# Kernel optimization log

Hardware: AMD Instinct MI355X
Metric: run time of the kernel (lower is better)

## Reference

```python
import jax, jax.numpy as jnp
import numpy as np

N_ENT = 50000
N_REL = 500
IN_DIM = 128
OUT_DIM = 128
N_EDGES = 500000
LRELU_SLOPE = 0.01  # torch F.leaky_relu default


def setup_inputs() -> dict:
    key = jax.random.key(0)
    ks = jax.random.split(key, 8)
    # triplets [3, E]: row0=src entity, row1=relation, row2=dst entity.
    # Ensure every entity appears as a source so no 0/0 in the edge-softmax division.
    src_extra = jax.random.randint(ks[0], (N_EDGES - N_ENT,), 0, N_ENT)
    src = jnp.concatenate([jnp.arange(N_ENT), src_extra])
    rel = jax.random.randint(ks[1], (N_EDGES,), 0, N_REL)
    dst = jax.random.randint(ks[2], (N_EDGES,), 0, N_ENT)
    triplets = jnp.stack([src, rel, dst]).astype(jnp.int64)
    ent_embed = jax.random.normal(ks[3], (N_ENT, IN_DIM), dtype=jnp.float32)
    rel_embed = jax.random.normal(ks[4], (N_REL, IN_DIM), dtype=jnp.float32)
    adj = jax.random.randint(ks[5], (2, N_EDGES), 0, N_ENT).astype(jnp.int64)  # unused by forward
    # Xavier-normal (gain=1.414) init for the two linear layers, like the torch module.
    std_a = 1.414 * np.sqrt(2.0 / (3 * IN_DIM + OUT_DIM))
    std_a2 = 1.414 * np.sqrt(2.0 / (OUT_DIM + 1))
    W_a = jax.random.normal(ks[6], (3 * IN_DIM, OUT_DIM), dtype=jnp.float32) * std_a
    b_a = jnp.zeros((OUT_DIM,), dtype=jnp.float32)
    W_a2 = jax.random.normal(ks[7], (OUT_DIM, 1), dtype=jnp.float32) * std_a2
    b_a2 = jnp.zeros((1,), dtype=jnp.float32)
    return {"triplets": triplets, "ent_embed": ent_embed, "rel_embed": rel_embed,
            "adj": adj, "W_a": W_a, "b_a": b_a, "W_a2": W_a2, "b_a2": b_a2}


def reference(triplets, ent_embed, rel_embed, adj, W_a, b_a, W_a2, b_a2):
    src, rel, dst = triplets[0], triplets[1], triplets[2]
    n_ent = ent_embed.shape[0]
    # Gather + concat: [E, 3*in_dim]
    h = jnp.concatenate([ent_embed[src], rel_embed[rel], ent_embed[dst]], axis=1)
    c = h @ W_a + b_a                                   # [E, out_dim]
    b = jax.nn.leaky_relu(c @ W_a2 + b_a2, LRELU_SLOPE)  # [E, 1]
    e_b = jnp.exp(b)                                    # [E, 1]
    # Sparse edge-softmax grouped by source node (sparse.sum over dst dim).
    denom = jax.ops.segment_sum(e_b, src, num_segments=n_ent)        # [N, 1]
    numer = jax.ops.segment_sum(e_b * c, src, num_segments=n_ent)    # [N, out_dim]
    out = numer / denom
    return jax.nn.elu(out)  # concat=True branch
```

## Files before the change

kernel.cpp:

```cpp
#include <hip/hip_runtime.h>

#define DIM 128

typedef __attribute__((ext_vector_type(8))) short bf16x8;
typedef __attribute__((ext_vector_type(4))) float f32x4;

__device__ inline unsigned short to_bf16(float f) {
    unsigned u = __float_as_uint(f);
    u = (u + 0x7FFFu + ((u >> 16) & 1u)) >> 16;
    return (unsigned short)u;
}
__device__ inline unsigned pack_bf16(float lo, float hi) {
    return (unsigned)to_bf16(lo) | ((unsigned)to_bf16(hi) << 16);
}
__device__ inline float unpack_lo(unsigned v) { return __uint_as_float(v << 16); }
__device__ inline float unpack_hi(unsigned v) { return __uint_as_float(v & 0xFFFF0000u); }

__global__ void wprep_kernel(const float* __restrict__ W_a, unsigned short* __restrict__ Wt,
                             int* __restrict__ counts, int n) {
    const int c = blockIdx.x;
    const int k = threadIdx.x;
    const int srow = (c < 128) ? k : (256 + k);
    const int scol = (c < 128) ? c : (c - 128);
    Wt[c * DIM + k] = to_bf16(W_a[srow * DIM + scol]);
    for (int i = blockIdx.x * 128 + k; i < n; i += 256 * 128) counts[i] = 0;
}

__global__ __launch_bounds__(256, 4) void stage1_kernel(
        const float* __restrict__ ent, const float* __restrict__ rel,
        const int* __restrict__ T, const unsigned short* __restrict__ Wt,
        const float* __restrict__ W_rel, const float* __restrict__ b_a,
        const float* __restrict__ Wa2,
        unsigned* __restrict__ P1h, unsigned* __restrict__ P3h, unsigned* __restrict__ P2h,
        float* __restrict__ q1, float* __restrict__ q3, float* __restrict__ q2,
        int* __restrict__ counts, int NE, int NR, int E, int GB, int HB, int RB) {
    __shared__ unsigned smem[8320];
    int b = blockIdx.x;
    const int t = threadIdx.x;

    if (b < GB) {
        const int half = b & 1;
        const int mrow = (b >> 1) * 128;

        #pragma unroll 4
        for (int i = 0; i < 16; ++i) {
            const int idx = i * 256 + t;
            const int row = idx >> 5;
            const int f4  = idx & 31;
            const int rg  = min(mrow + row, NE - 1);
            const float4 u = *(const float4*)(ent + (size_t)rg * DIM + f4 * 4);
            const unsigned d0 = pack_bf16(u.x, u.y);
            const unsigned d1 = pack_bf16(u.z, u.w);
            const int dw = (f4 * 2) ^ ((row & 7) << 2);
            *(uint2*)&smem[row * 64 + dw] = make_uint2(d0, d1);
        }
        __syncthreads();

        const int wv = t >> 6, lane = t & 63;
        const int g = lane >> 4, m = lane & 15;
        const unsigned short* Wh = Wt + half * 128 * DIM;

        f32x4 acc[2][8];
        #pragma unroll
        for (int rt = 0; rt < 2; ++rt)
            #pragma unroll
            for (int ct = 0; ct < 8; ++ct) acc[rt][ct] = (f32x4){0.f, 0.f, 0.f, 0.f};

        #pragma unroll
        for (int kk = 0; kk < 4; ++kk) {
            const int dwa = (kk * 16 + g * 4) ^ ((m & 7) << 2);
            const bf16x8 a0 = *(const bf16x8*)&smem[(wv * 32 + m) * 64 + dwa];
            const bf16x8 a1 = *(const bf16x8*)&smem[(wv * 32 + 16 + m) * 64 + dwa];
            #pragma unroll
            for (int ct = 0; ct < 8; ++ct) {
                const bf16x8 bb = *(const bf16x8*)(Wh + (ct * 16 + m) * DIM + kk * 32 + g * 8);
                acc[0][ct] = __builtin_amdgcn_mfma_f32_16x16x32_bf16(a0, bb, acc[0][ct], 0, 0, 0);
                acc[1][ct] = __builtin_amdgcn_mfma_f32_16x16x32_bf16(a1, bb, acc[1][ct], 0, 0, 0);
            }
        }
        __syncthreads();

        unsigned* __restrict__ Ph = half ? P3h : P1h;
        float*    __restrict__ qo = half ? q3  : q1;
        unsigned short* lds16 = (unsigned short*)smem;

        #pragma unroll
        for (int rt = 0; rt < 2; ++rt) {
            float qp[4] = {0.f, 0.f, 0.f, 0.f};
            #pragma unroll
            for (int ct = 0; ct < 8; ++ct) {
                const int c = ct * 16 + m;
                const float bias = half ? 0.0f : b_a[c];
                const float wa2  = Wa2[c];
                #pragma unroll
                for (int r = 0; r < 4; ++r) {
                    const float v = acc[rt][ct][r] + bias;
                    qp[r] += v * wa2;
                    lds16[(wv * 32 + rt * 16 + g * 4 + r) * 130 + c] = to_bf16(v);
                }
            }
            #pragma unroll
            for (int r = 0; r < 4; ++r) {
                float v = qp[r];
                #pragma unroll
                for (int o = 1; o < 16; o <<= 1) v += __shfl_xor(v, o);
                const int row = mrow + wv * 32 + rt * 16 + g * 4 + r;
                if (m == 0 && row < NE) qo[row] = v;
            }
        }
        __syncthreads();
        for (int i = 0; i < 32; ++i) {
            const int linear = i * 256 + t;
            const int row = linear >> 6, d = linear & 63;
            const int rg = mrow + row;
            if (rg < NE) Ph[(size_t)rg * 64 + d] = smem[row * 65 + d];
        }
        return;
    }
    b -= GB;

    if (b < HB) {
        for (int e = b * 256 + t; e < E; e += HB * 256)
            atomicAdd(&counts[T[e]], 1);
        return;
    }
    b -= HB;

    {
        float* xs   = (float*)smem;
        float* sred = (float*)(smem + 1024);
        const int row0 = b * 8;
        const int half = t >> 7;
        const int tc   = t & 127;
        #pragma unroll
        for (int e = 0; e < 4; ++e) {
            int row = row0 + half * 4 + e;
            xs[(half * 4 + e) * DIM + tc] = (row < NR) ? rel[(size_t)row * DIM + tc] : 0.0f;
        }
        __syncthreads();
        float acc[4] = {0.f, 0.f, 0.f, 0.f};
        #pragma unroll 4
        for (int k = 0; k < DIM; ++k) {
            const float wv = W_rel[k * DIM + tc];
            #pragma unroll
            for (int e = 0; e < 4; ++e) acc[e] += xs[(half * 4 + e) * DIM + k] * wv;
        }
        const float wa2 = Wa2[tc];
        const int lane = t & 63;
        #pragma unroll
        for (int e = 0; e < 4; ++e) {
            float v = acc[e] * wa2;
            #pragma unroll
            for (int o = 32; o > 0; o >>= 1) v += __shfl_down(v, o);
            if (lane == 0) sred[(half * 4 + e) * 2 + ((t >> 6) & 1)] = v;
        }
        __syncthreads();
        #pragma unroll
        for (int e = 0; e < 4; ++e) {
            int row = row0 + half * 4 + e;
            float hi = __shfl_down(acc[e], 1);
            if (row < NR && (tc & 1) == 0)
                P2h[(size_t)row * 64 + (tc >> 1)] = pack_bf16(acc[e], hi);
        }
        if (t < 8) {
            int row = row0 + t;
            if (row < NR) q2[row] = sred[t * 2] + sred[t * 2 + 1];
        }
    }
}

__device__ inline int wave_incl_scan(int v) {
    const int lane = threadIdx.x & 63;
    #pragma unroll
    for (int o = 1; o < 64; o <<= 1) {
        int u = __shfl_up(v, o);
        if (lane >= o) v += u;
    }
    return v;
}

__global__ void scan_bsum_kernel(const int* __restrict__ counts, int* __restrict__ bsum, int n) {
    const int t = threadIdx.x;
    const int base = blockIdx.x * 1024 + t * 4;
    int s = 0;
    #pragma unroll
    for (int j = 0; j < 4; ++j) if (base + j < n) s += counts[base + j];
    #pragma unroll
    for (int o = 32; o > 0; o >>= 1) s += __shfl_down(s, o);
    __shared__ int ws[4];
    if ((t & 63) == 0) ws[t >> 6] = s;
    __syncthreads();
    if (t == 0) bsum[blockIdx.x] = ws[0] + ws[1] + ws[2] + ws[3];
}

__global__ void scan_write_kernel(const int* __restrict__ counts, const int* __restrict__ bsum,
                                  int* __restrict__ offsets, int* __restrict__ cursor,
                                  int n, int total, int nb) {
    __shared__ int s_boff;
    __shared__ int wsum[4], wpre[4];
    const int t = threadIdx.x;
    if (t < 64) {
        int v = (t < nb) ? bsum[t] : 0;
        int incl = wave_incl_scan(v);
        int ex = incl - v;
        int want = __shfl(ex, (int)blockIdx.x);
        if (t == 0) s_boff = want;
    }
    const int base = blockIdx.x * 1024 + t * 4;
    int c[4];
    int s = 0;
    #pragma unroll
    for (int j = 0; j < 4; ++j) {
        c[j] = (base + j < n) ? counts[base + j] : 0;
        s += c[j];
    }
    int incl = wave_incl_scan(s);
    const int wid = t >> 6, lane = t & 63;
    if (lane == 63) wsum[wid] = incl;
    __syncthreads();
    if (t == 0) {
        int run = 0;
        #pragma unroll
        for (int k = 0; k < 4; ++k) { wpre[k] = run; run += wsum[k]; }
    }
    __syncthreads();
    int run = incl - s + wpre[wid] + s_boff;
    #pragma unroll
    for (int j = 0; j < 4; ++j) {
        if (base + j < n) { offsets[base + j] = run; cursor[base + j] = run; run += c[j]; }
    }
    if (base == 0 && blockIdx.x == 0) offsets[n] = total;
}

__global__ void scatter_kernel(const int* __restrict__ T, const float* __restrict__ q1,
                               const float* __restrict__ q2, const float* __restrict__ q3,
                               const float* __restrict__ b_a2, int* __restrict__ cursor,
                               uint2* __restrict__ rdw, int E) {
    const int e = blockIdx.x * blockDim.x + threadIdx.x;
    if (e >= E) return;
    const int s = T[e], r = T[E + e], d = T[2 * E + e];
    float b = q1[s] + q2[r] + q3[d] + b_a2[0];
    b = (b > 0.0f) ? b : 0.01f * b;
    const float wv = __expf(b);
    const int pos = atomicAdd(&cursor[s], 1);
    rdw[pos] = make_uint2(((unsigned)r << 17) | (unsigned)d, __float_as_uint(wv));
}

__global__ void gather_kernel(const int* __restrict__ offsets, const uint2* __restrict__ rdw,
                              const unsigned* __restrict__ P1h, const unsigned* __restrict__ P2h,
                              const unsigned* __restrict__ P3h, float* __restrict__ out, int n) {
    const int node = (blockIdx.x << 2) + (threadIdx.x >> 6);
    if (node >= n) return;
    const int lane = threadIdx.x & 63;
    const int lo = offsets[node], hi = offsets[node + 1];
    float axp[4] = {0.f,0.f,0.f,0.f};
    float ayp[4] = {0.f,0.f,0.f,0.f};
    float wsp[4] = {0.f,0.f,0.f,0.f};
    int i = lo;
    for (; i + 3 < hi; i += 4) {
        uint2 e[4];
        #pragma unroll
        for (int j = 0; j < 4; ++j) e[j] = rdw[i + j];
        unsigned v2[4], v3[4];
        #pragma unroll
        for (int j = 0; j < 4; ++j) {
            v2[j] = P2h[(size_t)(e[j].x >> 17) * 64 + lane];
            v3[j] = P3h[(size_t)(e[j].x & 0x1FFFFu) * 64 + lane];
        }
        #pragma unroll
        for (int j = 0; j < 4; ++j) {
            const float wv = __uint_as_float(e[j].y);
            axp[j] += wv * (unpack_lo(v2[j]) + unpack_lo(v3[j]));
            ayp[j] += wv * (unpack_hi(v2[j]) + unpack_hi(v3[j]));
            wsp[j] += wv;
        }
    }
    for (; i < hi; ++i) {
        const uint2 e0 = rdw[i];
        const unsigned v2a = P2h[(size_t)(e0.x >> 17) * 64 + lane];
        const unsigned v3a = P3h[(size_t)(e0.x & 0x1FFFFu) * 64 + lane];
        const float wv = __uint_as_float(e0.y);
        axp[0] += wv * (unpack_lo(v2a) + unpack_lo(v3a));
        ayp[0] += wv * (unpack_hi(v2a) + unpack_hi(v3a));
        wsp[0] += wv;
    }
    const float ax = (axp[0] + axp[1]) + (axp[2] + axp[3]);
    const float ay = (ayp[0] + ayp[1]) + (ayp[2] + ayp[3]);
    const float inv = 1.0f / ((wsp[0] + wsp[1]) + (wsp[2] + wsp[3]));
    const unsigned p1 = P1h[(size_t)node * 64 + lane];
    float v0 = unpack_lo(p1) + ax * inv;
    float v1 = unpack_hi(p1) + ay * inv;
    v0 = (v0 > 0.0f) ? v0 : (__expf(v0) - 1.0f);
    v1 = (v1 > 0.0f) ? v1 : (__expf(v1) - 1.0f);
    *(float2*)(out + (size_t)node * DIM + (lane << 1)) = make_float2(v0, v1);
}

extern "C" void kernel_launch(void* const* d_in, const int* in_sizes, int n_in,
                              void* d_out, int out_size, void* d_ws, size_t ws_size,
                              hipStream_t stream) {
    const int*   T    = (const int*)d_in[0];
    const float* ent  = (const float*)d_in[1];
    const float* rel  = (const float*)d_in[2];
    const float* W_a  = (const float*)d_in[4];
    const float* b_a  = (const float*)d_in[5];
    const float* W_a2 = (const float*)d_in[6];
    const float* b_a2 = (const float*)d_in[7];
    float* out = (float*)d_out;

    const int E  = in_sizes[0] / 3;
    const int NE = in_sizes[1] / DIM;
    const int NR = in_sizes[2] / DIM;
    const int NB = (NE + 1023) / 1024;
    const int GB = ((NE + 127) / 128) * 2;
    const int HB = 256;
    const int RB = (NR + 7) / 8;

    float* ws = (float*)d_ws;
    size_t off = 0;
    unsigned* P1h = (unsigned*)(ws + off); off += (size_t)NE * 64;
    unsigned* P3h = (unsigned*)(ws + off); off += (size_t)NE * 64;
    unsigned* P2h = (unsigned*)(ws + off); off += (size_t)NR * 64;
    unsigned short* Wt = (unsigned short*)(ws + off); off += 256 * DIM / 2;
    float* q1   = ws + off; off += NE;
    float* q3   = ws + off; off += NE;
    float* q2   = ws + off; off += NR + 64;
    int* counts  = (int*)(ws + off); off += NE;
    int* offsets = (int*)(ws + off); off += NE + 64;
    int* cursor  = (int*)(ws + off); off += NE;
    int* bsum    = (int*)(ws + off); off += 64;
    uint2* rdw   = (uint2*)(ws + off); off += (size_t)E * 2;

    wprep_kernel<<<256, 128, 0, stream>>>(W_a, Wt, counts, NE);

    stage1_kernel<<<GB + HB + RB, 256, 0, stream>>>(
        ent, rel, T, Wt, W_a + 128 * DIM, b_a, W_a2,
        P1h, P3h, P2h, q1, q3, q2, counts, NE, NR, E, GB, HB, RB);

    scan_bsum_kernel<<<NB, 256, 0, stream>>>(counts, bsum, NE);
    scan_write_kernel<<<NB, 256, 0, stream>>>(counts, bsum, offsets, cursor, NE, E, NB);

    scatter_kernel<<<(E + 255) / 256, 256, 0, stream>>>(T, q1, q2, q3, b_a2, cursor, rdw, E);

    gather_kernel<<<(NE + 3) / 4, 256, 0, stream>>>(offsets, rdw, P1h, P2h, P3h, out, NE);
}
```

Measured before the change: 111.8 us.

## Split fused stage1 into separate GEMM and histogram/relation kernels, restage W in LDS

The fused stage1 kernel is split into a 512-thread GEMM kernel and a separate histogram-plus-relation-projection kernel. The GEMM now stages the weight half in LDS and loads A fragments straight from global memory into registers, where before the entity tile went through LDS and weights came from global. Each wave now computes 16 rows instead of 32. This is meant to cut repeated global reads of the weights and shorten the fused kernel's critical path. The cost is an extra kernel launch, and the histogram no longer overlaps with the GEMM.

```diff
diff --git a/kernel.cpp b/kernel.cpp
--- a/kernel.cpp
+++ b/kernel.cpp
@@ -26,98 +26,105 @@
     for (int i = blockIdx.x * 128 + k; i < n; i += 256 * 128) counts[i] = 0;
 }
 
-__global__ __launch_bounds__(256, 4) void stage1_kernel(
-        const float* __restrict__ ent, const float* __restrict__ rel,
-        const int* __restrict__ T, const unsigned short* __restrict__ Wt,
-        const float* __restrict__ W_rel, const float* __restrict__ b_a,
-        const float* __restrict__ Wa2,
-        unsigned* __restrict__ P1h, unsigned* __restrict__ P3h, unsigned* __restrict__ P2h,
-        float* __restrict__ q1, float* __restrict__ q3, float* __restrict__ q2,
-        int* __restrict__ counts, int NE, int NR, int E, int GB, int HB, int RB) {
+__global__ __launch_bounds__(512) void gemm_kernel(
+        const float* __restrict__ ent, const unsigned short* __restrict__ Wt,
+        const float* __restrict__ b_a, const float* __restrict__ Wa2,
+        unsigned* __restrict__ P1h, unsigned* __restrict__ P3h,
+        float* __restrict__ q1, float* __restrict__ q3, int NE) {
     __shared__ unsigned smem[8320];
+    const int b = blockIdx.x;
+    const int half = b & 1;
+    const int mrow = (b >> 1) * 128;
+    const int t = threadIdx.x;
+    const int wv = t >> 6;
+    const int lane = t & 63;
+    const int g = lane >> 4, m = lane & 15;
+
+    const unsigned short* Wh = Wt + half * 128 * DIM;
+    #pragma unroll
+    for (int i = 0; i < 4; ++i) {
+        const int ci  = i * 8 + wv;
+        const int row = ci * 4 + (lane >> 4);
+        const int dw0 = (lane & 15) * 4;
+        const int sdw = dw0 ^ ((row & 7) << 2);
+        const uint4 v = *(const uint4*)(Wh + row * DIM + sdw * 2);
+        *(uint4*)&smem[ci * 256 + lane * 4] = v;
+    }
+
+    const int rowA = min(mrow + wv * 16 + m, NE - 1);
+    const float* arow = ent + (size_t)rowA * DIM;
+    bf16x8 afrag[4];
+    #pragma unroll
+    for (int kk = 0; kk < 4; ++kk) {
+        const float4 u0 = *(const float4*)(arow + kk * 32 + g * 8);
+        const float4 u1 = *(const float4*)(arow + kk * 32 + g * 8 + 4);
+        bf16x8 a;
+        a[0] = (short)to_bf16(u0.x); a[1] = (short)to_bf16(u0.y);
+        a[2] = (short)to_bf16(u0.z); a[3] = (short)to_bf16(u0.w);
+        a[4] = (short)to_bf16(u1.x); a[5] = (short)to_bf16(u1.y);
+        a[6] = (short)to_bf16(u1.z); a[7] = (short)to_bf16(u1.w);
+        afrag[kk] = a;
+    }
+    __syncthreads();
+
+    f32x4 acc[8];
+    #pragma unroll
+    for (int ct = 0; ct < 8; ++ct) acc[ct] = (f32x4){0.f, 0.f, 0.f, 0.f};
+    #pragma unroll
+    for (int kk = 0; kk < 4; ++kk) {
+        #pragma unroll
+        for (int ct = 0; ct < 8; ++ct) {
+            const int dw = (kk * 16 + g * 4) ^ ((m & 7) << 2);
+            const bf16x8 bb = *(const bf16x8*)&smem[(ct * 16 + m) * 64 + dw];
+            acc[ct] = __builtin_amdgcn_mfma_f32_16x16x32_bf16(afrag[kk], bb, acc[ct], 0, 0, 0);
+        }
+    }
+    __syncthreads();
+
+    unsigned* __restrict__ Ph = half ? P3h : P1h;
+    float*    __restrict__ qo = half ? q3  : q1;
+    unsigned short* lds16 = (unsigned short*)smem;
+
+    float qp[4] = {0.f, 0.f, 0.f, 0.f};
+    #pragma unroll
+    for (int ct = 0; ct < 8; ++ct) {
+        const int c = ct * 16 + m;
+        const float bias = half ? 0.0f : b_a[c];
+        const float wa2  = Wa2[c];
+        #pragma unroll
+        for (int r = 0; r < 4; ++r) {
+            const float v = acc[ct][r] + bias;
+            qp[r] += v * wa2;
+            lds16[(wv * 16 + g * 4 + r) * 130 + c] = to_bf16(v);
+        }
+    }
+    #pragma unroll
+    for (int r = 0; r < 4; ++r) {
+        float v = qp[r];
+        #pragma unroll
+        for (int o = 1; o < 16; o <<= 1) v += __shfl_xor(v, o);
+        const int row = mrow + wv * 16 + g * 4 + r;
+        if (m == 0 && row < NE) qo[row] = v;
+    }
+    __syncthreads();
+    #pragma unroll 4
+    for (int i = 0; i < 16; ++i) {
+        const int linear = i * 512 + t;
+        const int row = linear >> 6, d = linear & 63;
+        const int rg = mrow + row;
+        if (rg < NE) Ph[(size_t)rg * 64 + d] = smem[row * 65 + d];
+    }
+}
+
+__global__ __launch_bounds__(256) void histrel_kernel(
+        const float* __restrict__ rel, const int* __restrict__ T,
+        const float* __restrict__ W_rel, const float* __restrict__ Wa2,
+        unsigned* __restrict__ P2h, float* __restrict__ q2,
+        int* __restrict__ counts, int NR, int E, int HB) {
+    __shared__ float xs[8 * DIM];
+    __shared__ float sred[16];
     int b = blockIdx.x;
     const int t = threadIdx.x;
-
-    if (b < GB) {
-        const int half = b & 1;
-        const int mrow = (b >> 1) * 128;
-
-        #pragma unroll 4
-        for (int i = 0; i < 16; ++i) {
-            const int idx = i * 256 + t;
-            const int row = idx >> 5;
-            const int f4  = idx & 31;
-            const int rg  = min(mrow + row, NE - 1);
-            const float4 u = *(const float4*)(ent + (size_t)rg * DIM + f4 * 4);
-            const unsigned d0 = pack_bf16(u.x, u.y);
-            const unsigned d1 = pack_bf16(u.z, u.w);
-            const int dw = (f4 * 2) ^ ((row & 7) << 2);
-            *(uint2*)&smem[row * 64 + dw] = make_uint2(d0, d1);
-        }
-        __syncthreads();
-
-        const int wv = t >> 6, lane = t & 63;
-        const int g = lane >> 4, m = lane & 15;
-        const unsigned short* Wh = Wt + half * 128 * DIM;
-
-        f32x4 acc[2][8];
-        #pragma unroll
-        for (int rt = 0; rt < 2; ++rt)
-            #pragma unroll
-            for (int ct = 0; ct < 8; ++ct) acc[rt][ct] = (f32x4){0.f, 0.f, 0.f, 0.f};
-
-        #pragma unroll
-        for (int kk = 0; kk < 4; ++kk) {
-            const int dwa = (kk * 16 + g * 4) ^ ((m & 7) << 2);
-            const bf16x8 a0 = *(const bf16x8*)&smem[(wv * 32 + m) * 64 + dwa];
-            const bf16x8 a1 = *(const bf16x8*)&smem[(wv * 32 + 16 + m) * 64 + dwa];
-            #pragma unroll
-            for (int ct = 0; ct < 8; ++ct) {
-                const bf16x8 bb = *(const bf16x8*)(Wh + (ct * 16 + m) * DIM + kk * 32 + g * 8);
-                acc[0][ct] = __builtin_amdgcn_mfma_f32_16x16x32_bf16(a0, bb, acc[0][ct], 0, 0, 0);
-                acc[1][ct] = __builtin_amdgcn_mfma_f32_16x16x32_bf16(a1, bb, acc[1][ct], 0, 0, 0);
-            }
-        }
-        __syncthreads();
-
-        unsigned* __restrict__ Ph = half ? P3h : P1h;
-        float*    __restrict__ qo = half ? q3  : q1;
-        unsigned short* lds16 = (unsigned short*)smem;
-
-        #pragma unroll
-        for (int rt = 0; rt < 2; ++rt) {
-            float qp[4] = {0.f, 0.f, 0.f, 0.f};
-            #pragma unroll
-            for (int ct = 0; ct < 8; ++ct) {
-                const int c = ct * 16 + m;
-                const float bias = half ? 0.0f : b_a[c];
-                const float wa2  = Wa2[c];
-                #pragma unroll
-                for (int r = 0; r < 4; ++r) {
-                    const float v = acc[rt][ct][r] + bias;
-                    qp[r] += v * wa2;
-                    lds16[(wv * 32 + rt * 16 + g * 4 + r) * 130 + c] = to_bf16(v);
-                }
-            }
-            #pragma unroll
-            for (int r = 0; r < 4; ++r) {
-                float v = qp[r];
-                #pragma unroll
-                for (int o = 1; o < 16; o <<= 1) v += __shfl_xor(v, o);
-                const int row = mrow + wv * 32 + rt * 16 + g * 4 + r;
-                if (m == 0 && row < NE) qo[row] = v;
-            }
-        }
-        __syncthreads();
-        for (int i = 0; i < 32; ++i) {
-            const int linear = i * 256 + t;
-            const int row = linear >> 6, d = linear & 63;
-            const int rg = mrow + row;
-            if (rg < NE) Ph[(size_t)rg * 64 + d] = smem[row * 65 + d];
-        }
-        return;
-    }
-    b -= GB;
 
     if (b < HB) {
         for (int e = b * 256 + t; e < E; e += HB * 256)
@@ -126,46 +133,42 @@
     }
     b -= HB;
 
-    {
-        float* xs   = (float*)smem;
-        float* sred = (float*)(smem + 1024);
-        const int row0 = b * 8;
-        const int half = t >> 7;
-        const int tc   = t & 127;
-        #pragma unroll
-        for (int e = 0; e < 4; ++e) {
-            int row = row0 + half * 4 + e;
-            xs[(half * 4 + e) * DIM + tc] = (row < NR) ? rel[(size_t)row * DIM + tc] : 0.0f;
-        }
-        __syncthreads();
-        float acc[4] = {0.f, 0.f, 0.f, 0.f};
-        #pragma unroll 4
-        for (int k = 0; k < DIM; ++k) {
-            const float wv = W_rel[k * DIM + tc];
-            #pragma unroll
-            for (int e = 0; e < 4; ++e) acc[e] += xs[(half * 4 + e) * DIM + k] * wv;
-        }
-        const float wa2 = Wa2[tc];
-        const int lane = t & 63;
-        #pragma unroll
-        for (int e = 0; e < 4; ++e) {
-            float v = acc[e] * wa2;
-            #pragma unroll
-            for (int o = 32; o > 0; o >>= 1) v += __shfl_down(v, o);
-            if (lane == 0) sred[(half * 4 + e) * 2 + ((t >> 6) & 1)] = v;
-        }
-        __syncthreads();
-        #pragma unroll
-        for (int e = 0; e < 4; ++e) {
-            int row = row0 + half * 4 + e;
-            float hi = __shfl_down(acc[e], 1);
-            if (row < NR && (tc & 1) == 0)
-                P2h[(size_t)row * 64 + (tc >> 1)] = pack_bf16(acc[e], hi);
-        }
-        if (t < 8) {
-            int row = row0 + t;
-            if (row < NR) q2[row] = sred[t * 2] + sred[t * 2 + 1];
-        }
+    const int row0 = b * 8;
+    const int half = t >> 7;
+    const int tc   = t & 127;
+    #pragma unroll
+    for (int e = 0; e < 4; ++e) {
+        int row = row0 + half * 4 + e;
+        xs[(half * 4 + e) * DIM + tc] = (row < NR) ? rel[(size_t)row * DIM + tc] : 0.0f;
+    }
+    __syncthreads();
+    float acc[4] = {0.f, 0.f, 0.f, 0.f};
+    #pragma unroll 4
+    for (int k = 0; k < DIM; ++k) {
+        const float wv = W_rel[k * DIM + tc];
+        #pragma unroll
+        for (int e = 0; e < 4; ++e) acc[e] += xs[(half * 4 + e) * DIM + k] * wv;
+    }
+    const float wa2 = Wa2[tc];
+    const int lane = t & 63;
+    #pragma unroll
+    for (int e = 0; e < 4; ++e) {
+        float v = acc[e] * wa2;
+        #pragma unroll
+        for (int o = 32; o > 0; o >>= 1) v += __shfl_down(v, o);
+        if (lane == 0) sred[(half * 4 + e) * 2 + ((t >> 6) & 1)] = v;
+    }
+    __syncthreads();
+    #pragma unroll
+    for (int e = 0; e < 4; ++e) {
+        int row = row0 + half * 4 + e;
+        float hi = __shfl_down(acc[e], 1);
+        if (row < NR && (tc & 1) == 0)
+            P2h[(size_t)row * 64 + (tc >> 1)] = pack_bf16(acc[e], hi);
+    }
+    if (t < 8) {
+        int row = row0 + t;
+        if (row < NR) q2[row] = sred[t * 2] + sred[t * 2 + 1];
     }
 }
 
@@ -332,9 +335,10 @@
 
     wprep_kernel<<<256, 128, 0, stream>>>(W_a, Wt, counts, NE);
 
-    stage1_kernel<<<GB + HB + RB, 256, 0, stream>>>(
-        ent, rel, T, Wt, W_a + 128 * DIM, b_a, W_a2,
-        P1h, P3h, P2h, q1, q3, q2, counts, NE, NR, E, GB, HB, RB);
+    gemm_kernel<<<GB, 512, 0, stream>>>(ent, Wt, b_a, W_a2, P1h, P3h, q1, q3, NE);
+
+    histrel_kernel<<<HB + RB, 256, 0, stream>>>(rel, T, W_a + 128 * DIM, W_a2,
+                                                P2h, q2, counts, NR, E, HB);
 
     scan_bsum_kernel<<<NB, 256, 0, stream>>>(counts, bsum, NE);
     scan_write_kernel<<<NB, 256, 0, stream>>>(counts, bsum, offsets, cursor, NE, E, NB);
```

Result: slower. 118.7 us (+6.2%).
